# Optimization experiments

Hardware: AMD Instinct MI355X
Metric: run time of the kernel (lower is better)

The kernel has to match this reference:

```python
import jax, jax.numpy as jnp
import numpy as np

IN_DIM = 512
HID = IN_DIM // 2
N_SCENES = 64
SEG_LEN = 4096
N = N_SCENES * SEG_LEN
EPS = 1e-5


def setup_inputs() -> dict:
    key = jax.random.key(0)
    ks = jax.random.split(key, 6)
    feats = jax.random.normal(ks[0], (N, IN_DIM), dtype=jnp.float32)
    offsets = (jnp.arange(N_SCENES + 1, dtype=jnp.int32) * SEG_LEN)
    ln_g = jnp.ones((IN_DIM,), jnp.float32) + 0.02 * jax.random.normal(ks[1], (IN_DIM,), jnp.float32)
    ln_b = 0.02 * jax.random.normal(ks[2], (IN_DIM,), jnp.float32)
    w1 = jax.random.normal(ks[3], (HID, IN_DIM), jnp.float32) / np.sqrt(IN_DIM)
    b1 = jnp.zeros((HID,), jnp.float32)
    w2 = jax.random.normal(ks[4], (1, HID), jnp.float32) / np.sqrt(HID)
    b2 = jnp.zeros((1,), jnp.float32)
    return {"feats": feats, "ln_g": ln_g, "ln_b": ln_b, "w1": w1, "b1": b1, "w2": w2, "b2": b2, "offsets": offsets}


def reference(feats, ln_g, ln_b, w1, b1, w2, b2, offsets):
    n = feats.shape[0]
    # segment id per point from prefix-sum offsets
    seg = jnp.searchsorted(offsets, jnp.arange(n, dtype=offsets.dtype), side="right") - 1
    # score MLP: LayerNorm -> Linear -> GELU(exact) -> Linear -> scalar
    mu = jnp.mean(feats, axis=-1, keepdims=True)
    var = jnp.mean(jnp.square(feats - mu), axis=-1, keepdims=True)
    x = (feats - mu) * jax.lax.rsqrt(var + EPS) * ln_g + ln_b
    h = jax.nn.gelu(x @ w1.T + b1, approximate=False)  # [N, HID]
    s = (h @ w2.T + b2)[:, 0]  # [N]
    # segment softmax (stable)
    smax = jax.ops.segment_max(s, seg, num_segments=N_SCENES)
    e = jnp.exp(s - smax[seg])
    denom = jax.ops.segment_sum(e, seg, num_segments=N_SCENES)
    w = e / denom[seg]
    # weighted sum per segment -> [N_SCENES, IN_DIM]
    pooled = jax.ops.segment_sum(feats * w[:, None], seg, num_segments=N_SCENES)
    return pooled
```

## Files before the change

### kernel.cpp

```cpp
#include <hip/hip_runtime.h>

#define IN_DIM 512
#define HID_DIM 256
#define ROWS 64
#define XSS 520
#define PSEG 8
#define PSTRIDE 516

typedef __bf16 bf16x8 __attribute__((ext_vector_type(8)));
typedef unsigned short ushort8 __attribute__((ext_vector_type(8)));
typedef float floatx16 __attribute__((ext_vector_type(16)));

__device__ __forceinline__ unsigned short f2bf_rne(float x) {
    unsigned int u = __float_as_uint(x);
    u += 0x7FFFu + ((u >> 16) & 1u);
    return (unsigned short)(u >> 16);
}
__device__ __forceinline__ unsigned int pack_bf2(float lo, float hi) {
    const unsigned int u0 = __float_as_uint(lo) + 0x8000u;
    const unsigned int u1 = __float_as_uint(hi) + 0x8000u;
    return __builtin_amdgcn_perm(u1, u0, 0x07060302u);
}
__device__ __forceinline__ float gelu(float x) {
    const float ax = fabsf(x) * 0.70710678118654752f;
    const float t = __builtin_amdgcn_rcpf(1.0f + 0.3275911f * ax);
    const float y = t * (0.254829592f +
                    t * (-0.284496736f +
                    t * (1.421413741f +
                    t * (-1.453152027f + t * 1.061405429f))));
    const float e = __expf(-ax * ax);
    float er = 1.0f - y * e;
    er = __builtin_copysignf(er, x);
    return 0.5f * x * (1.0f + er);
}

__device__ __forceinline__ void barrier_nodrain() {
    asm volatile("s_waitcnt lgkmcnt(0)" ::: "memory");
    __builtin_amdgcn_sched_barrier(0);
    __builtin_amdgcn_s_barrier();
    __builtin_amdgcn_sched_barrier(0);
}

__global__ void prep_w1_kernel(const float* __restrict__ w1, const float* __restrict__ ln_g,
                               const float* __restrict__ ln_b, const float* __restrict__ b1,
                               unsigned short* __restrict__ w1g, float* __restrict__ gw,
                               float* __restrict__ c1) {
    const int wid = threadIdx.x >> 6;
    const int lane = threadIdx.x & 63;
    const int h = blockIdx.x * 4 + wid;
    const int c8 = lane * 8;
    const float4 wv0 = *(const float4*)(w1 + (size_t)h * IN_DIM + c8);
    const float4 wv1 = *(const float4*)(w1 + (size_t)h * IN_DIM + c8 + 4);
    const float4 g0 = *(const float4*)(ln_g + c8);
    const float4 g1 = *(const float4*)(ln_g + c8 + 4);
    const float4 bb0 = *(const float4*)(ln_b + c8);
    const float4 bb1 = *(const float4*)(ln_b + c8 + 4);
    float wg[8] = {wv0.x * g0.x, wv0.y * g0.y, wv0.z * g0.z, wv0.w * g0.w,
                   wv1.x * g1.x, wv1.y * g1.y, wv1.z * g1.z, wv1.w * g1.w};
    float sg = wg[0] + wg[1] + wg[2] + wg[3] + wg[4] + wg[5] + wg[6] + wg[7];
    float sb = wv0.x * bb0.x + wv0.y * bb0.y + wv0.z * bb0.z + wv0.w * bb0.w +
               wv1.x * bb1.x + wv1.y * bb1.y + wv1.z * bb1.z + wv1.w * bb1.w;
    ushort8 outv;
#pragma unroll
    for (int j = 0; j < 8; j++) outv[j] = f2bf_rne(wg[j]);
    *(ushort8*)(w1g + (size_t)h * IN_DIM + c8) = outv;
    for (int m = 32; m; m >>= 1) {
        sg += __shfl_xor(sg, m);
        sb += __shfl_xor(sb, m);
    }
    if (lane == 0) {
        gw[h] = sg;
        c1[h] = sb + b1[h];
    }
}

__global__ __launch_bounds__(512)
__attribute__((amdgpu_waves_per_eu(4, 4))) void fused_kernel(
    const float* __restrict__ feats, const unsigned short* __restrict__ w1g,
    const float* __restrict__ gw, const float* __restrict__ c1,
    const float* __restrict__ w2, const float* __restrict__ b2,
    const int* __restrict__ offsets, float* __restrict__ partials, int N) {
    __shared__ unsigned short xs[ROWS][XSS];
    __shared__ float spart[8][ROWS];
    __shared__ float2 stats_s[ROWS];

    const int tid = threadIdx.x;
    const int wid = tid >> 6;
    const int lane = tid & 63;
    const int l31 = lane & 31;
    const int hi = lane >> 5;
    const int seg = blockIdx.x / PSEG;
    const int part = blockIdx.x % PSEG;
    const int st = offsets[seg];
    const int en = offsets[seg + 1];
    const int len = en - st;
    const int chunk = (len + PSEG - 1) / PSEG;
    const int rs = st + part * chunk;
    const int re = min(rs + chunk, en);
    const int nt = (re > rs) ? ((re - rs + ROWS - 1) / ROWS) : 0;

    const int hid = wid * 32 + l31;
    const float gw0 = gw[hid];
    const float c10 = c1[hid];
    const float w20 = w2[hid];
    const float b2v = b2[0];

    const int srow = tid >> 5;
    const int sc = tid & 31;

    float O = 0.0f;
    float Mreg = -3.0e38f, Dreg = 0.0f;

    auto issue = [&](float4 (&v)[4], int rowq) {
        int rg = rowq + srow;
        if (rg > N - 1) rg = N - 1;
        const float* fp = feats + (size_t)rg * IN_DIM + sc * 4;
#pragma unroll
        for (int j = 0; j < 4; j++) v[j] = *(const float4*)(fp + j * 128);
    };
    auto process = [&](const float4 (&v)[4], int lrow0) {
        float sf = 0.0f, qf = 0.0f;
#pragma unroll
        for (int j = 0; j < 4; j++) {
            sf += v[j].x + v[j].y + v[j].z + v[j].w;
            qf = fmaf(v[j].x, v[j].x, qf);
            qf = fmaf(v[j].y, v[j].y, qf);
            qf = fmaf(v[j].z, v[j].z, qf);
            qf = fmaf(v[j].w, v[j].w, qf);
        }
#pragma unroll
        for (int j = 0; j < 4; j++) {
            uint2 pk;
            pk.x = pack_bf2(v[j].x, v[j].y);
            pk.y = pack_bf2(v[j].z, v[j].w);
            *(uint2*)&xs[lrow0 + srow][sc * 4 + j * 128] = pk;
        }
        sf += __shfl_xor(sf, 1);  qf += __shfl_xor(qf, 1);
        sf += __shfl_xor(sf, 2);  qf += __shfl_xor(qf, 2);
        sf += __shfl_xor(sf, 4);  qf += __shfl_xor(qf, 4);
        sf += __shfl_xor(sf, 8);  qf += __shfl_xor(qf, 8);
        sf += __shfl_xor(sf, 16); qf += __shfl_xor(qf, 16);
        if (sc == 0) {
            const float mu = sf * (1.0f / IN_DIM);
            const float var = fmaxf(qf * (1.0f / IN_DIM) - mu * mu, 0.0f);
            stats_s[lrow0 + srow] = make_float2(mu, rsqrtf(var + 1e-5f));
        }
    };

    float4 f[4], g[4], h[4];
    if (nt > 0) issue(f, rs);

    for (int t = 0; t < nt; t++) {
        const int row0 = rs + t * ROWS;

        issue(g, row0 + 16);
        issue(h, row0 + 32);
        process(f, 0);
        issue(f, row0 + 48);
        process(g, 16);
        process(h, 32);
        process(f, 48);
        __syncthreads();

        floatx16 acc0 = (floatx16)(0.0f);
        floatx16 acc1 = (floatx16)(0.0f);
        {
            const unsigned short* bp = w1g + (size_t)hid * IN_DIM + hi * 8;
            const unsigned short* ap0 = &xs[l31][hi * 8];
            const unsigned short* ap1 = &xs[32 + l31][hi * 8];
            ushort8 br[8];
#pragma unroll
            for (int i = 0; i < 8; i++) br[i] = *(const ushort8*)(bp + i * 16);
#pragma unroll
            for (int kg = 0; kg < 4; kg++) {
#pragma unroll
                for (int u = 0; u < 8; u++) {
                    const int ki = kg * 8 + u;
                    const bf16x8 a0 = __builtin_bit_cast(bf16x8, *(const ushort8*)(ap0 + ki * 16));
                    const bf16x8 a1 = __builtin_bit_cast(bf16x8, *(const ushort8*)(ap1 + ki * 16));
                    const bf16x8 bv = __builtin_bit_cast(bf16x8, br[u]);
                    acc0 = __builtin_amdgcn_mfma_f32_32x32x16_bf16(a0, bv, acc0, 0, 0, 0);
                    acc1 = __builtin_amdgcn_mfma_f32_32x32x16_bf16(a1, bv, acc1, 0, 0, 0);
                    if (ki + 8 < 32)
                        br[u] = *(const ushort8*)(bp + (ki + 8) * 16);
                }
            }
        }

        {
            float tv[16];
#pragma unroll
            for (int q = 0; q < 16; q++) {
                const int rowl = (q & 3) + 8 * (q >> 2) + 4 * hi;
                const float2 stt = stats_s[rowl];
                const float hh = stt.y * (acc0[q] - stt.x * gw0) + c10;
                tv[q] = gelu(hh) * w20;
            }
#pragma unroll
            for (int m = 1; m < 32; m <<= 1)
#pragma unroll
                for (int q = 0; q < 16; q++) tv[q] += __shfl_xor(tv[q], m);
            if (l31 == 0) {
#pragma unroll
                for (int q = 0; q < 16; q++)
                    spart[wid][(q & 3) + 8 * (q >> 2) + 4 * hi] = tv[q];
            }
#pragma unroll
            for (int q = 0; q < 16; q++) {
                const int rowl = 32 + (q & 3) + 8 * (q >> 2) + 4 * hi;
                const float2 stt = stats_s[rowl];
                const float hh = stt.y * (acc1[q] - stt.x * gw0) + c10;
                tv[q] = gelu(hh) * w20;
            }
#pragma unroll
            for (int m = 1; m < 32; m <<= 1)
#pragma unroll
                for (int q = 0; q < 16; q++) tv[q] += __shfl_xor(tv[q], m);
            if (l31 == 0) {
#pragma unroll
                for (int q = 0; q < 16; q++)
                    spart[wid][32 + (q & 3) + 8 * (q >> 2) + 4 * hi] = tv[q];
            }
        }

        if (t + 1 < nt) issue(f, row0 + ROWS);
        barrier_nodrain();

        float wv_, al;
        {
            float sv = spart[0][lane] + spart[1][lane] + spart[2][lane] + spart[3][lane] +
                       spart[4][lane] + spart[5][lane] + spart[6][lane] + spart[7][lane] + b2v;
            if (row0 + lane >= re) sv = -3.0e38f;
            float mt = sv;
#pragma unroll
            for (int m = 1; m < 64; m <<= 1) mt = fmaxf(mt, __shfl_xor(mt, m));
            const float Mnew = fmaxf(Mreg, mt);
            al = __expf(Mreg - Mnew);
            wv_ = __expf(sv - Mnew);
            float ws = wv_;
#pragma unroll
            for (int m = 1; m < 64; m <<= 1) ws += __shfl_xor(ws, m);
            Dreg = Dreg * al + ws;
            Mreg = Mnew;
        }

        O *= al;
#pragma unroll 16
        for (int rr = 0; rr < ROWS; rr++) {
            const float wr = __shfl(wv_, rr);
            const unsigned int us = (unsigned int)xs[rr][tid];
            O = fmaf(wr, __uint_as_float(us << 16), O);
        }
        if (t + 1 < nt) barrier_nodrain();
    }

    float* pp = partials + (size_t)blockIdx.x * PSTRIDE;
    pp[tid] = O;
    if (tid == 0) {
        pp[512] = Mreg;
        pp[513] = Dreg;
    }
}

__global__ void combine_kernel(const float* __restrict__ partials, float* __restrict__ out) {
    const int seg = blockIdx.x;
    const int t = threadIdx.x;
    const float* base = partials + (size_t)seg * PSEG * PSTRIDE;
    float M = -3.0e38f;
#pragma unroll
    for (int p = 0; p < PSEG; p++) M = fmaxf(M, base[p * PSTRIDE + 512]);
    float D = 0.0f, a0 = 0.0f, a1 = 0.0f;
#pragma unroll
    for (int p = 0; p < PSEG; p++) {
        const float e = __expf(base[p * PSTRIDE + 512] - M);
        D += e * base[p * PSTRIDE + 513];
        a0 += e * base[p * PSTRIDE + 2 * t];
        a1 += e * base[p * PSTRIDE + 2 * t + 1];
    }
    out[(size_t)seg * IN_DIM + 2 * t] = a0 / D;
    out[(size_t)seg * IN_DIM + 2 * t + 1] = a1 / D;
}

extern "C" void kernel_launch(void* const* d_in, const int* in_sizes, int n_in,
                              void* d_out, int out_size, void* d_ws, size_t ws_size,
                              hipStream_t stream) {
    const float* feats = (const float*)d_in[0];
    const float* ln_g = (const float*)d_in[1];
    const float* ln_b = (const float*)d_in[2];
    const float* w1 = (const float*)d_in[3];
    const float* b1 = (const float*)d_in[4];
    const float* w2 = (const float*)d_in[5];
    const float* b2 = (const float*)d_in[6];
    const int* offsets = (const int*)d_in[7];
    const int N = in_sizes[0] / IN_DIM;
    const int nseg = in_sizes[7] - 1;
    float* out = (float*)d_out;

    char* ws = (char*)d_ws;
    unsigned short* w1g = (unsigned short*)ws;
    float* gw = (float*)(ws + (size_t)HID_DIM * IN_DIM * 2);
    float* c1 = gw + HID_DIM;
    float* partials = c1 + HID_DIM;

    prep_w1_kernel<<<HID_DIM / 4, 256, 0, stream>>>(w1, ln_g, ln_b, b1, w1g, gw, c1);
    fused_kernel<<<nseg * PSEG, 512, 0, stream>>>(feats, w1g, gw, c1, w2, b2, offsets,
                                                  partials, N);
    combine_kernel<<<nseg, 256, 0, stream>>>(partials, out);
}
```

Baseline: 985.5 us.

## Cut register pressure: serialize MFMA halves, shrink prefetch, split pooled accumulation by rows

```diff
diff --git a/kernel.cpp b/kernel.cpp
--- a/kernel.cpp
+++ b/kernel.cpp
@@ -74,8 +74,7 @@
     }
 }
 
-__global__ __launch_bounds__(512)
-__attribute__((amdgpu_waves_per_eu(4, 4))) void fused_kernel(
+__global__ __launch_bounds__(512, 4) void fused_kernel(
     const float* __restrict__ feats, const unsigned short* __restrict__ w1g,
     const float* __restrict__ gw, const float* __restrict__ c1,
     const float* __restrict__ w2, const float* __restrict__ b2,
@@ -108,7 +107,10 @@
     const int srow = tid >> 5;
     const int sc = tid & 31;
 
-    float O = 0.0f;
+    const int pc = (tid & 255) * 2;
+    const int rhalf = tid >> 8;
+
+    float O0 = 0.0f, O1 = 0.0f;
     float Mreg = -3.0e38f, Dreg = 0.0f;
 
     auto issue = [&](float4 (&v)[4], int rowq) {
@@ -147,53 +149,52 @@
         }
     };
 
-    float4 f[4], g[4], h[4];
-    if (nt > 0) issue(f, rs);
+    float4 f[4], g[4];
+    if (nt > 0) {
+        issue(f, rs);
+        issue(g, rs + 16);
+    }
 
     for (int t = 0; t < nt; t++) {
         const int row0 = rs + t * ROWS;
 
-        issue(g, row0 + 16);
-        issue(h, row0 + 32);
         process(f, 0);
-        issue(f, row0 + 48);
+        issue(f, row0 + 32);
         process(g, 16);
-        process(h, 32);
-        process(f, 48);
+        issue(g, row0 + 48);
+        process(f, 32);
+        process(g, 48);
         __syncthreads();
 
-        floatx16 acc0 = (floatx16)(0.0f);
-        floatx16 acc1 = (floatx16)(0.0f);
-        {
-            const unsigned short* bp = w1g + (size_t)hid * IN_DIM + hi * 8;
-            const unsigned short* ap0 = &xs[l31][hi * 8];
-            const unsigned short* ap1 = &xs[32 + l31][hi * 8];
-            ushort8 br[8];
-#pragma unroll
-            for (int i = 0; i < 8; i++) br[i] = *(const ushort8*)(bp + i * 16);
-#pragma unroll
-            for (int kg = 0; kg < 4; kg++) {
-#pragma unroll
-                for (int u = 0; u < 8; u++) {
-                    const int ki = kg * 8 + u;
-                    const bf16x8 a0 = __builtin_bit_cast(bf16x8, *(const ushort8*)(ap0 + ki * 16));
-                    const bf16x8 a1 = __builtin_bit_cast(bf16x8, *(const ushort8*)(ap1 + ki * 16));
-                    const bf16x8 bv = __builtin_bit_cast(bf16x8, br[u]);
-                    acc0 = __builtin_amdgcn_mfma_f32_32x32x16_bf16(a0, bv, acc0, 0, 0, 0);
-                    acc1 = __builtin_amdgcn_mfma_f32_32x32x16_bf16(a1, bv, acc1, 0, 0, 0);
-                    if (ki + 8 < 32)
-                        br[u] = *(const ushort8*)(bp + (ki + 8) * 16);
+#pragma unroll 1
+        for (int h2 = 0; h2 < 2; ++h2) {
+            floatx16 acc = (floatx16)(0.0f);
+            {
+                const unsigned short* bp = w1g + (size_t)hid * IN_DIM + hi * 8;
+                const unsigned short* ap = &xs[h2 * 32 + l31][hi * 8];
+                ushort8 br[8];
+#pragma unroll
+                for (int i = 0; i < 8; i++) br[i] = *(const ushort8*)(bp + i * 16);
+#pragma unroll
+                for (int kg = 0; kg < 4; kg++) {
+#pragma unroll
+                    for (int u = 0; u < 8; u++) {
+                        const int ki = kg * 8 + u;
+                        const bf16x8 a =
+                            __builtin_bit_cast(bf16x8, *(const ushort8*)(ap + ki * 16));
+                        const bf16x8 bv = __builtin_bit_cast(bf16x8, br[u]);
+                        acc = __builtin_amdgcn_mfma_f32_32x32x16_bf16(a, bv, acc, 0, 0, 0);
+                        if (ki + 8 < 32)
+                            br[u] = *(const ushort8*)(bp + (ki + 8) * 16);
+                    }
                 }
             }
-        }
-
-        {
             float tv[16];
 #pragma unroll
             for (int q = 0; q < 16; q++) {
-                const int rowl = (q & 3) + 8 * (q >> 2) + 4 * hi;
+                const int rowl = h2 * 32 + (q & 3) + 8 * (q >> 2) + 4 * hi;
                 const float2 stt = stats_s[rowl];
-                const float hh = stt.y * (acc0[q] - stt.x * gw0) + c10;
+                const float hh = stt.y * (acc[q] - stt.x * gw0) + c10;
                 tv[q] = gelu(hh) * w20;
             }
 #pragma unroll
@@ -203,27 +204,14 @@
             if (l31 == 0) {
 #pragma unroll
                 for (int q = 0; q < 16; q++)
-                    spart[wid][(q & 3) + 8 * (q >> 2) + 4 * hi] = tv[q];
+                    spart[wid][h2 * 32 + (q & 3) + 8 * (q >> 2) + 4 * hi] = tv[q];
             }
-#pragma unroll
-            for (int q = 0; q < 16; q++) {
-                const int rowl = 32 + (q & 3) + 8 * (q >> 2) + 4 * hi;
-                const float2 stt = stats_s[rowl];
-                const float hh = stt.y * (acc1[q] - stt.x * gw0) + c10;
-                tv[q] = gelu(hh) * w20;
-            }
-#pragma unroll
-            for (int m = 1; m < 32; m <<= 1)
-#pragma unroll
-                for (int q = 0; q < 16; q++) tv[q] += __shfl_xor(tv[q], m);
-            if (l31 == 0) {
-#pragma unroll
-                for (int q = 0; q < 16; q++)
-                    spart[wid][32 + (q & 3) + 8 * (q >> 2) + 4 * hi] = tv[q];
-            }
-        }
-
-        if (t + 1 < nt) issue(f, row0 + ROWS);
+        }
+
+        if (t + 1 < nt) {
+            issue(f, row0 + ROWS);
+            issue(g, row0 + ROWS + 16);
+        }
         barrier_nodrain();
 
         float wv_, al;
@@ -244,18 +232,31 @@
             Mreg = Mnew;
         }
 
-        O *= al;
-#pragma unroll 16
-        for (int rr = 0; rr < ROWS; rr++) {
+        O0 *= al;
+        O1 *= al;
+#pragma unroll 8
+        for (int r = 0; r < 32; r++) {
+            const int rr = rhalf * 32 + r;
             const float wr = __shfl(wv_, rr);
-            const unsigned int us = (unsigned int)xs[rr][tid];
-            O = fmaf(wr, __uint_as_float(us << 16), O);
+            const unsigned int d = *(const unsigned int*)&xs[rr][pc];
+            O0 = fmaf(wr, __uint_as_float(d << 16), O0);
+            O1 = fmaf(wr, __uint_as_float(d & 0xffff0000u), O1);
         }
         if (t + 1 < nt) barrier_nodrain();
     }
 
+    __syncthreads();
+    float* mrg = (float*)spart;
+    if (rhalf == 1) {
+        mrg[pc] = O0;
+        mrg[pc + 1] = O1;
+    }
+    __syncthreads();
     float* pp = partials + (size_t)blockIdx.x * PSTRIDE;
-    pp[tid] = O;
+    if (rhalf == 0) {
+        pp[pc] = O0 + mrg[pc];
+        pp[pc + 1] = O1 + mrg[pc + 1];
+    }
     if (tid == 0) {
         pp[512] = Mreg;
         pp[513] = Dreg;
```

New measurement: 963.9 us. 2.2% less time.
